# Kernel tuning notes

Hardware: AMD Instinct MI355X
Metric: run time of the kernel (lower is better)

Reference implementation:

```python
import jax, jax.numpy as jnp
import numpy as np

N = 20000      # nodes per side
E = 160000     # edges
C = 512        # input_channels
C_OUT = 512    # output_channels
TEMP = float(np.sqrt(C))  # self.temperature = sqrt(input_channels)
NEG_SLOPE = 0.01          # LeakyReLU default


def _xavier(key, shape):
    fan_in, fan_out = shape[1], shape[0]
    std = np.sqrt(2.0 / (fan_in + fan_out))
    return jax.random.normal(key, shape, dtype=jnp.float32) * std


def setup_inputs() -> dict:
    key = jax.random.key(0)
    ks = jax.random.split(key, 10)
    return {
        "node_left": jax.random.normal(ks[0], (N, C), dtype=jnp.float32),
        "segmentation_index_left": jax.random.randint(ks[1], (E,), 0, N),
        "index_left": jax.random.randint(ks[2], (E,), 0, N),
        "node_right": jax.random.normal(ks[3], (N, C), dtype=jnp.float32),
        "segmentation_index_right": jax.random.randint(ks[4], (E,), 0, N),
        "index_right": jax.random.randint(ks[5], (E,), 0, N),
        "Wk": _xavier(ks[6], (C, C)),      # key_projection.weight
        "Wv": _xavier(ks[7], (C, C)),      # value_projection.weight
        "Wo": _xavier(ks[8], (C_OUT, C)),  # out_projection Linear weight
        "bo": jnp.zeros((C_OUT,), dtype=jnp.float32),
    }


def segment_softmax(scores, seg_idx, num_segments, temperature):
    # numerically stable softmax over variable-length segments of edges
    s = scores / temperature
    m = jax.ops.segment_max(s, seg_idx, num_segments=num_segments)
    m = jnp.where(jnp.isneginf(m), 0.0, m)  # guard empty segments
    e = jnp.exp(s - m[seg_idx])
    z = jax.ops.segment_sum(e, seg_idx, num_segments=num_segments)
    return e / z[seg_idx]


def _message(translation, seg_idx, num_segments, neighbor, Wo, bo):
    attn = segment_softmax(translation, seg_idx, num_segments, TEMP)  # [E]
    # dropout is identity at inference
    msg = jax.ops.segment_sum(attn[:, None] * neighbor, seg_idx,
                              num_segments=num_segments)  # [N, C]
    h = msg @ Wo.T + bo
    return jnp.where(h >= 0, h, NEG_SLOPE * h)  # LeakyReLU


def reference(node_left, segmentation_index_left, index_left,
              node_right, segmentation_index_right, index_right,
              Wk, Wv, Wo, bo):
    n_left = node_left.shape[0]
    n_right = node_right.shape[0]
    # key projections gathered to edges
    left_center = (node_left @ Wk.T)[segmentation_index_left]    # [E, C]
    right_center = (node_right @ Wk.T)[segmentation_index_right]  # [E, C]
    # value projections gathered to edges (cross side)
    left_neighbor = (node_right @ Wv.T)[segmentation_index_right]  # [E, C]
    right_neighbor = (node_left @ Wv.T)[segmentation_index_left]   # [E, C]
    translation = jnp.sum(left_center * right_center, axis=1)      # [E]
    msg_left = _message(translation, segmentation_index_left, n_left,
                        left_neighbor, Wo, bo)
    msg_right = _message(translation, segmentation_index_right, n_right,
                         right_neighbor, Wo, bo)
    return (msg_left, msg_right)
```

## Files before the change

### kernel.cpp

```cpp
#include <hip/hip_runtime.h>


#define C_DIM 512
#define TEMP_INV (1.0f / 22.627416997969522f)

using bf16x8 = __attribute__((ext_vector_type(8))) __bf16;
using s16x8  = __attribute__((ext_vector_type(8))) short;
using s16x4  = __attribute__((ext_vector_type(4))) short;
using f32x4  = __attribute__((ext_vector_type(4))) float;

__device__ __forceinline__ float bf2f(short u) {
    union { unsigned u; float f; } t;
    t.u = ((unsigned)(unsigned short)u) << 16;
    return t.f;
}
__device__ __forceinline__ short f2bf(float f) {
    union { float f; unsigned u; } t;
    t.f = f;
    unsigned r = t.u + 0x7FFFu + ((t.u >> 16) & 1u);
    return (short)(r >> 16);
}

__global__ void cvt2_f32_bf16(const float* __restrict__ inA,
                              const float* __restrict__ inB,
                              short* __restrict__ out, long n4half) {
    long i = (long)blockIdx.x * blockDim.x + threadIdx.x;
    long stride = (long)gridDim.x * blockDim.x;
    long n4 = 2 * n4half;
    for (; i < n4; i += stride) {
        const float4* src = (i < n4half)
            ? reinterpret_cast<const float4*>(inA) + i
            : reinterpret_cast<const float4*>(inB) + (i - n4half);
        float4 v = *src;
        s16x4 o;
        o[0] = f2bf(v.x); o[1] = f2bf(v.y); o[2] = f2bf(v.z); o[3] = f2bf(v.w);
        reinterpret_cast<s16x4*>(out)[i] = o;
    }
}

__global__ void cvt_weights(const float* __restrict__ Wk,
                            const float* __restrict__ Wv,
                            const float* __restrict__ Wo,
                            short* __restrict__ Wkc, short* __restrict__ WoB,
                            short* __restrict__ WvT) {
    int b = blockIdx.x;
    int tid = threadIdx.x;
    if (b < 64) {
        __shared__ float t[64][65];
        int bx = b & 7, by = b >> 3;
#pragma unroll
        for (int i = 0; i < 4; ++i) {
            int idx = i * 256 + tid;
            int row = idx >> 4, c4 = idx & 15;
            float4 v = *(const float4*)&Wv[(size_t)(by * 64 + row) * 512 + bx * 64 + c4 * 4];
            t[row][c4 * 4 + 0] = v.x; t[row][c4 * 4 + 1] = v.y;
            t[row][c4 * 4 + 2] = v.z; t[row][c4 * 4 + 3] = v.w;
        }
        __syncthreads();
#pragma unroll
        for (int i = 0; i < 4; ++i) {
            int idx = i * 256 + tid;
            int row = idx >> 4, g = idx & 15;
            s16x4 o;
            o[0] = f2bf(t[g * 4 + 0][row]);
            o[1] = f2bf(t[g * 4 + 1][row]);
            o[2] = f2bf(t[g * 4 + 2][row]);
            o[3] = f2bf(t[g * 4 + 3][row]);
            *(s16x4*)&WvT[(size_t)(bx * 64 + row) * 512 + by * 64 + g * 4] = o;
        }
    } else {
        const float* src = (b < 128) ? Wk : Wo;
        short* dst = (b < 128) ? Wkc : WoB;
        long base = (long)(b & 63) * 1024;
#pragma unroll
        for (int i = 0; i < 4; ++i) {
            long idx = base + i * 256 + tid;
            float4 v = reinterpret_cast<const float4*>(src)[idx];
            s16x4 o;
            o[0] = f2bf(v.x); o[1] = f2bf(v.y); o[2] = f2bf(v.z); o[3] = f2bf(v.w);
            reinterpret_cast<s16x4*>(dst)[idx] = o;
        }
    }
}

__global__ __launch_bounds__(256, 3)
void gemm_bt(const short* __restrict__ A, const short* __restrict__ B,
             short* __restrict__ Cp, int M, int N, int K, int nn, int total) {
    __shared__ short As[3][128 * 32];
    __shared__ short Bs[3][128 * 32];

    const int bid = blockIdx.x;
    const int q = total >> 3, r = total & 7;
    const int xcd = bid & 7, idx = bid >> 3;
    const int swz = (xcd < r ? xcd * (q + 1) : r * (q + 1) + (xcd - r) * q) + idx;
    const int bm = (swz / nn) * 128;
    const int bn = (swz % nn) * 128;

    const int tid  = threadIdx.x;
    const int lane = tid & 63;
    const int wid  = tid >> 6;
    const int wm   = (wid >> 1) * 64;
    const int wn   = (wid & 1) * 64;
    const int lrow  = lane & 15;
    const int khalf = lane >> 4;

    auto stage = [&](short* dA, short* dB, int k0) {
#pragma unroll
        for (int j = 0; j < 2; ++j) {
            int L    = j * 256 + tid;
            int pr   = L >> 3;
            int slot = L & 7;
            int g    = slot ^ (pr & 7);
            int row  = pr * 2 + (g >> 2);
            int kg   = g & 3;
            int wb   = (j * 256 + (tid & ~63)) * 16;
            {
                int grow = bm + row; if (grow >= M) grow = M - 1;
                const short* src = A + (size_t)grow * K + k0 + kg * 8;
                __builtin_amdgcn_global_load_lds(
                    (__attribute__((address_space(1))) void*)src,
                    (__attribute__((address_space(3))) void*)((char*)dA + wb),
                    16, 0, 0);
            }
            {
                int grow = bn + row; if (grow >= N) grow = N - 1;
                const short* src = B + (size_t)grow * K + k0 + kg * 8;
                __builtin_amdgcn_global_load_lds(
                    (__attribute__((address_space(1))) void*)src,
                    (__attribute__((address_space(3))) void*)((char*)dB + wb),
                    16, 0, 0);
            }
        }
    };

    auto frag = [&](const short* h, int row) -> bf16x8 {
        int pr   = row >> 1;
        int g    = ((row & 1) << 2) | khalf;
        int slot = g ^ (pr & 7);
        return *(const bf16x8*)&h[pr * 64 + slot * 8];
    };

    f32x4 acc[4][4] = {};
    const int nt = K >> 5;

    stage(As[0], Bs[0], 0);
    stage(As[1], Bs[1], 32);

    for (int t = 0; t < nt; ++t) {
        const unsigned cur = (unsigned)t % 3u;
        if (t + 2 < nt) {
            const unsigned nxt = (unsigned)(t + 2) % 3u;
            stage(As[nxt], Bs[nxt], (t + 2) << 5);
            asm volatile("s_waitcnt vmcnt(8)" ::: "memory");
        } else if (t + 1 < nt) {
            asm volatile("s_waitcnt vmcnt(4)" ::: "memory");
        } else {
            asm volatile("s_waitcnt vmcnt(0)" ::: "memory");
        }
        __builtin_amdgcn_s_barrier();

        const short* as = As[cur];
        const short* bs = Bs[cur];
        bf16x8 af[4], bfr[4];
#pragma unroll
        for (int m = 0; m < 4; ++m) af[m] = frag(as, wm + m * 16 + lrow);
#pragma unroll
        for (int n = 0; n < 4; ++n) bfr[n] = frag(bs, wn + n * 16 + lrow);

        asm volatile("s_waitcnt lgkmcnt(0)" ::: "memory");
        __builtin_amdgcn_sched_barrier(0);
        __builtin_amdgcn_s_barrier();

        __builtin_amdgcn_s_setprio(1);
#pragma unroll
        for (int m = 0; m < 4; ++m)
#pragma unroll
            for (int n = 0; n < 4; ++n)
                acc[m][n] = __builtin_amdgcn_mfma_f32_16x16x32_bf16(
                    af[m], bfr[n], acc[m][n], 0, 0, 0);
        __builtin_amdgcn_s_setprio(0);
    }

    const int crow0 = (lane >> 4) * 4;
    const int ccol  = lane & 15;
#pragma unroll
    for (int m = 0; m < 4; ++m) {
#pragma unroll
        for (int n = 0; n < 4; ++n) {
            int col = bn + wn + n * 16 + ccol;
#pragma unroll
            for (int r2 = 0; r2 < 4; ++r2) {
                int row = bm + wm + m * 16 + crow0 + r2;
                if (row < M) Cp[(size_t)row * N + col] = f2bf(acc[m][n][r2]);
            }
        }
    }
}

__global__ void count_edges2(const int* __restrict__ segL, const int* __restrict__ segR,
                             int* __restrict__ cnt, int E, int N) {
    int i = blockIdx.x * blockDim.x + threadIdx.x;
    int st = gridDim.x * blockDim.x;
    for (; i < E; i += st) {
        atomicAdd(&cnt[segL[i]], 1);
        atomicAdd(&cnt[N + segR[i]], 1);
    }
}

__global__ void scan_blocks(const int* __restrict__ cnt, int* __restrict__ off,
                            int* __restrict__ bsum, int n) {
    __shared__ int ws[4];
    int tid = threadIdx.x, lane = tid & 63, wid = tid >> 6;
    int i = blockIdx.x * 256 + tid;
    int x = (i < n) ? cnt[i] : 0;
    int v = x;
#pragma unroll
    for (int d = 1; d < 64; d <<= 1) {
        int t = __shfl_up(v, d, 64);
        if (lane >= d) v += t;
    }
    if (lane == 63) ws[wid] = v;
    __syncthreads();
    int woff = 0;
    for (int w = 0; w < wid; ++w) woff += ws[w];
    v += woff;
    if (i < n) off[i + 1] = v;
    if (tid == 255) bsum[blockIdx.x] = v;
}

__global__ void scan_tops(int* __restrict__ bsum, int nb) {
    __shared__ int ws[4];
    int tid = threadIdx.x, lane = tid & 63, wid = tid >> 6;
    int x = (tid < nb) ? bsum[tid] : 0;
    int v = x;
#pragma unroll
    for (int d = 1; d < 64; d <<= 1) {
        int t = __shfl_up(v, d, 64);
        if (lane >= d) v += t;
    }
    if (lane == 63) ws[wid] = v;
    __syncthreads();
    int woff = 0;
    for (int w = 0; w < wid; ++w) woff += ws[w];
    v += woff;
    if (tid < nb) bsum[tid] = v - x;
}

__global__ void scan_apply(int* __restrict__ off, const int* __restrict__ bsum,
                           int* __restrict__ cnt, int n) {
    int i = blockIdx.x * 256 + threadIdx.x;
    if (i < n) {
        off[i + 1] += bsum[blockIdx.x];
        cnt[i] = 0;
    }
    if (i == 0) off[0] = 0;
}

__global__ void edge_dot_fill(const short* __restrict__ proj,
                              const int* __restrict__ segL, const int* __restrict__ segR,
                              const int* __restrict__ off, int* __restrict__ cur,
                              float2* __restrict__ pairs, int E, int N) {
    int e0 = blockIdx.x * 16 + (threadIdx.x >> 6) * 4;
    if (e0 >= E) return;
    int lane = threadIdx.x & 63;

    float sum[4];
#pragma unroll
    for (int k = 0; k < 4; ++k) {
        int ek = e0 + k; if (ek >= E) ek = e0;
        const short* a = proj + (size_t)segL[ek] * 1024 + lane * 8;
        const short* b = proj + (size_t)(N + segR[ek]) * 1024 + lane * 8;
        s16x8 va = *(const s16x8*)a;
        s16x8 vb = *(const s16x8*)b;
        float s = 0.f;
#pragma unroll
        for (int j = 0; j < 8; ++j) s += bf2f(va[j]) * bf2f(vb[j]);
        sum[k] = s;
    }
#pragma unroll
    for (int o = 32; o > 0; o >>= 1) {
#pragma unroll
        for (int k = 0; k < 4; ++k) sum[k] += __shfl_xor(sum[k], o, 64);
    }
    if (lane < 4) {
        int ek = e0 + lane;
        if (ek < E) {
            float s = (lane == 0) ? sum[0] : (lane == 1) ? sum[1]
                    : (lane == 2) ? sum[2] : sum[3];
            float we = __expf(s * TEMP_INV);
            int sl = segL[ek], sr = segR[ek];
            int pl = off[sl] + atomicAdd(&cur[sl], 1);
            pairs[pl] = make_float2(we, __int_as_float(N + sr));
            int pr = off[N + sr] + atomicAdd(&cur[N + sr], 1);
            pairs[pr] = make_float2(we, __int_as_float(sl));
        }
    }
}

__global__ void node_msg(const int* __restrict__ off,
                         const float2* __restrict__ pairs,
                         const short* __restrict__ proj,
                         const float* __restrict__ bo,
                         float* __restrict__ out, int NN2) {
    int n = blockIdx.x * 4 + (threadIdx.x >> 6);
    if (n >= NN2) return;
    int lane = threadIdx.x & 63;
    int beg = off[n], end = off[n + 1];
    const short* VW = proj + 512 + lane * 8;

    float acc[8] = {};
    float z = 0.f;
    int i = beg;
    for (; i + 3 < end; i += 4) {
        float2 p0 = pairs[i], p1 = pairs[i + 1];
        float2 p2 = pairs[i + 2], p3 = pairs[i + 3];
        const s16x8 v0 = *(const s16x8*)(VW + (size_t)__float_as_int(p0.y) * 1024);
        const s16x8 v1 = *(const s16x8*)(VW + (size_t)__float_as_int(p1.y) * 1024);
        const s16x8 v2 = *(const s16x8*)(VW + (size_t)__float_as_int(p2.y) * 1024);
        const s16x8 v3 = *(const s16x8*)(VW + (size_t)__float_as_int(p3.y) * 1024);
        z += (p0.x + p1.x) + (p2.x + p3.x);
#pragma unroll
        for (int j = 0; j < 8; ++j) {
            acc[j] += p0.x * bf2f(v0[j]) + p1.x * bf2f(v1[j]);
            acc[j] += p2.x * bf2f(v2[j]) + p3.x * bf2f(v3[j]);
        }
    }
    for (; i < end; ++i) {
        float2 p = pairs[i];
        const s16x8 v = *(const s16x8*)(VW + (size_t)__float_as_int(p.y) * 1024);
        z += p.x;
#pragma unroll
        for (int j = 0; j < 8; ++j) acc[j] += p.x * bf2f(v[j]);
    }
    float inv = (z > 0.f) ? 1.f / z : 0.f;

    float4 bs0 = *(const float4*)&bo[lane * 8];
    float4 bs1 = *(const float4*)&bo[lane * 8 + 4];
    float bb[8] = {bs0.x, bs0.y, bs0.z, bs0.w, bs1.x, bs1.y, bs1.z, bs1.w};
    f32x4 h0, h1;
#pragma unroll
    for (int j = 0; j < 4; ++j) {
        float v = acc[j] * inv + bb[j];
        h0[j] = v >= 0.f ? v : 0.01f * v;
    }
#pragma unroll
    for (int j = 0; j < 4; ++j) {
        float v = acc[4 + j] * inv + bb[4 + j];
        h1[j] = v >= 0.f ? v : 0.01f * v;
    }
    float* orow = out + (size_t)n * C_DIM + lane * 8;
    __builtin_nontemporal_store(h0, (f32x4*)&orow[0]);
    __builtin_nontemporal_store(h1, (f32x4*)&orow[4]);
}

extern "C" void kernel_launch(void* const* d_in, const int* in_sizes, int n_in,
                              void* d_out, int out_size, void* d_ws, size_t ws_size,
                              hipStream_t stream) {
    const float* node_left  = (const float*)d_in[0];
    const int*   segL       = (const int*)d_in[1];
    const float* node_right = (const float*)d_in[3];
    const int*   segR       = (const int*)d_in[4];
    const float* Wk         = (const float*)d_in[6];
    const float* Wv         = (const float*)d_in[7];
    const float* Wo         = (const float*)d_in[8];
    const float* bo         = (const float*)d_in[9];

    const int C = C_DIM;
    const int N = in_sizes[0] / C;
    const int E = in_sizes[1];
    const int NN2 = 2 * N;

    size_t offb = 0;
    auto alloc = [&](size_t bytes) -> void* {
        void* p = (char*)d_ws + offb;
        offb += (bytes + 255) & ~(size_t)255;
        return p;
    };
    short* nodeLR_b = (short*)alloc((size_t)NN2 * C * 2);
    short* Wkc_b  = (short*)alloc((size_t)1024 * C * 2);
    short* Wc_b   = Wkc_b + (size_t)C * C;
    short* Wo_b   = (short*)alloc((size_t)C * C * 2);
    short* WvT_b  = (short*)alloc((size_t)C * C * 2);
    short* proj   = (short*)alloc((size_t)NN2 * 1024 * 2);
    float2* pairs = (float2*)alloc((size_t)2 * E * 8);
    int* cnt  = (int*)alloc((size_t)NN2 * 4);
    int* off  = (int*)alloc((size_t)(NN2 + 1) * 4);
    int* bsum = (int*)alloc(256 * 4);

    const int nsb = (NN2 + 255) / 256;

    hipMemsetAsync(cnt, 0, (size_t)NN2 * 4, stream);
    count_edges2<<<512, 256, 0, stream>>>(segL, segR, cnt, E, N);
    scan_blocks<<<nsb, 256, 0, stream>>>(cnt, off, bsum, NN2);
    scan_tops<<<1, 256, 0, stream>>>(bsum, nsb);
    scan_apply<<<nsb, 256, 0, stream>>>(off, bsum, cnt, NN2);

    cvt2_f32_bf16<<<2048, 256, 0, stream>>>(node_left, node_right, nodeLR_b,
                                            (long)N * C / 4);
    cvt_weights<<<192, 256, 0, stream>>>(Wk, Wv, Wo, Wkc_b, Wo_b, WvT_b);

    gemm_bt<<<16, 256, 0, stream>>>(Wo_b, WvT_b, Wc_b, C, C, C, 4, 16);
    {
        int nm = (NN2 + 127) / 128, nn = 1024 / 128;
        int total = nm * nn;
        gemm_bt<<<total, 256, 0, stream>>>(nodeLR_b, Wkc_b, proj, NN2, 1024, C,
                                           nn, total);
    }

    edge_dot_fill<<<(E + 15) / 16, 256, 0, stream>>>(proj, segL, segR, off, cnt,
                                                     pairs, E, N);

    node_msg<<<(NN2 + 3) / 4, 256, 0, stream>>>(off, pairs, proj, bo,
                                                (float*)d_out, NN2);
}
```

Before: 230.1 us.

## Fold key projection into Gram matrix so only right side is projected

```diff
diff --git a/kernel.cpp b/kernel.cpp
--- a/kernel.cpp
+++ b/kernel.cpp
@@ -41,18 +41,21 @@
 __global__ void cvt_weights(const float* __restrict__ Wk,
                             const float* __restrict__ Wv,
                             const float* __restrict__ Wo,
-                            short* __restrict__ Wkc, short* __restrict__ WoB,
-                            short* __restrict__ WvT) {
+                            short* __restrict__ WkT, short* __restrict__ WvT,
+                            short* __restrict__ WoB) {
     int b = blockIdx.x;
     int tid = threadIdx.x;
-    if (b < 64) {
+    if (b < 128) {
+        const float* src = (b < 64) ? Wv : Wk;
+        short* dst = (b < 64) ? WvT : WkT;
+        int bb = b & 63;
         __shared__ float t[64][65];
-        int bx = b & 7, by = b >> 3;
+        int bx = bb & 7, by = bb >> 3;
 #pragma unroll
         for (int i = 0; i < 4; ++i) {
             int idx = i * 256 + tid;
             int row = idx >> 4, c4 = idx & 15;
-            float4 v = *(const float4*)&Wv[(size_t)(by * 64 + row) * 512 + bx * 64 + c4 * 4];
+            float4 v = *(const float4*)&src[(size_t)(by * 64 + row) * 512 + bx * 64 + c4 * 4];
             t[row][c4 * 4 + 0] = v.x; t[row][c4 * 4 + 1] = v.y;
             t[row][c4 * 4 + 2] = v.z; t[row][c4 * 4 + 3] = v.w;
         }
@@ -66,35 +69,40 @@
             o[1] = f2bf(t[g * 4 + 1][row]);
             o[2] = f2bf(t[g * 4 + 2][row]);
             o[3] = f2bf(t[g * 4 + 3][row]);
-            *(s16x4*)&WvT[(size_t)(bx * 64 + row) * 512 + by * 64 + g * 4] = o;
+            *(s16x4*)&dst[(size_t)(bx * 64 + row) * 512 + by * 64 + g * 4] = o;
         }
     } else {
-        const float* src = (b < 128) ? Wk : Wo;
-        short* dst = (b < 128) ? Wkc : WoB;
         long base = (long)(b & 63) * 1024;
 #pragma unroll
         for (int i = 0; i < 4; ++i) {
             long idx = base + i * 256 + tid;
-            float4 v = reinterpret_cast<const float4*>(src)[idx];
+            float4 v = reinterpret_cast<const float4*>(Wo)[idx];
             s16x4 o;
             o[0] = f2bf(v.x); o[1] = f2bf(v.y); o[2] = f2bf(v.z); o[3] = f2bf(v.w);
-            reinterpret_cast<s16x4*>(dst)[idx] = o;
-        }
-    }
-}
-
-__global__ __launch_bounds__(256, 3)
-void gemm_bt(const short* __restrict__ A, const short* __restrict__ B,
-             short* __restrict__ Cp, int M, int N, int K, int nn, int total) {
-    __shared__ short As[3][128 * 32];
-    __shared__ short Bs[3][128 * 32];
+            reinterpret_cast<s16x4*>(WoB)[idx] = o;
+        }
+    }
+}
+
+__global__ __launch_bounds__(256, 4)
+void gemm_dual(const short* __restrict__ A0, const short* __restrict__ B0,
+               short* __restrict__ C0, int M0, int t0,
+               const short* __restrict__ A1, const short* __restrict__ B1,
+               short* __restrict__ C1, int M1, int total) {
+    __shared__ short As[2][128 * 32];
+    __shared__ short Bs[2][128 * 32];
 
     const int bid = blockIdx.x;
     const int q = total >> 3, r = total & 7;
     const int xcd = bid & 7, idx = bid >> 3;
     const int swz = (xcd < r ? xcd * (q + 1) : r * (q + 1) + (xcd - r) * q) + idx;
-    const int bm = (swz / nn) * 128;
-    const int bn = (swz % nn) * 128;
+
+    const short* A; const short* B; short* Cp; int M; int tile;
+    if (swz < t0) { A = A0; B = B0; Cp = C0; M = M0; tile = swz; }
+    else          { A = A1; B = B1; Cp = C1; M = M1; tile = swz - t0; }
+    const int bm = (tile >> 2) * 128;
+    const int bn = (tile & 3) * 128;
+    const int K = C_DIM;
 
     const int tid  = threadIdx.x;
     const int lane = tid & 63;
@@ -123,7 +131,7 @@
                     16, 0, 0);
             }
             {
-                int grow = bn + row; if (grow >= N) grow = N - 1;
+                int grow = bn + row;
                 const short* src = B + (size_t)grow * K + k0 + kg * 8;
                 __builtin_amdgcn_global_load_lds(
                     (__attribute__((address_space(1))) void*)src,
@@ -144,15 +152,11 @@
     const int nt = K >> 5;
 
     stage(As[0], Bs[0], 0);
-    stage(As[1], Bs[1], 32);
 
     for (int t = 0; t < nt; ++t) {
-        const unsigned cur = (unsigned)t % 3u;
-        if (t + 2 < nt) {
-            const unsigned nxt = (unsigned)(t + 2) % 3u;
-            stage(As[nxt], Bs[nxt], (t + 2) << 5);
-            asm volatile("s_waitcnt vmcnt(8)" ::: "memory");
-        } else if (t + 1 < nt) {
+        const int cur = t & 1;
+        if (t + 1 < nt) {
+            stage(As[cur ^ 1], Bs[cur ^ 1], (t + 1) << 5);
             asm volatile("s_waitcnt vmcnt(4)" ::: "memory");
         } else {
             asm volatile("s_waitcnt vmcnt(0)" ::: "memory");
@@ -191,7 +195,7 @@
 #pragma unroll
             for (int r2 = 0; r2 < 4; ++r2) {
                 int row = bm + wm + m * 16 + crow0 + r2;
-                if (row < M) Cp[(size_t)row * N + col] = f2bf(acc[m][n][r2]);
+                if (row < M) Cp[(size_t)row * C_DIM + col] = f2bf(acc[m][n][r2]);
             }
         }
     }
@@ -256,7 +260,8 @@
     if (i == 0) off[0] = 0;
 }
 
-__global__ void edge_dot_fill(const short* __restrict__ proj,
+__global__ void edge_dot_fill(const short* __restrict__ KL,
+                              const short* __restrict__ KR,
                               const int* __restrict__ segL, const int* __restrict__ segR,
                               const int* __restrict__ off, int* __restrict__ cur,
                               float2* __restrict__ pairs, int E, int N) {
@@ -268,8 +273,8 @@
 #pragma unroll
     for (int k = 0; k < 4; ++k) {
         int ek = e0 + k; if (ek >= E) ek = e0;
-        const short* a = proj + (size_t)segL[ek] * 1024 + lane * 8;
-        const short* b = proj + (size_t)(N + segR[ek]) * 1024 + lane * 8;
+        const short* a = KL + (size_t)segL[ek] * 512 + lane * 8;
+        const short* b = KR + (size_t)segR[ek] * 512 + lane * 8;
         s16x8 va = *(const s16x8*)a;
         s16x8 vb = *(const s16x8*)b;
         float s = 0.f;
@@ -299,14 +304,14 @@
 
 __global__ void node_msg(const int* __restrict__ off,
                          const float2* __restrict__ pairs,
-                         const short* __restrict__ proj,
+                         const short* __restrict__ VW,
                          const float* __restrict__ bo,
                          float* __restrict__ out, int NN2) {
     int n = blockIdx.x * 4 + (threadIdx.x >> 6);
     if (n >= NN2) return;
     int lane = threadIdx.x & 63;
     int beg = off[n], end = off[n + 1];
-    const short* VW = proj + 512 + lane * 8;
+    const short* VWp = VW + lane * 8;
 
     float acc[8] = {};
     float z = 0.f;
@@ -314,10 +319,10 @@
     for (; i + 3 < end; i += 4) {
         float2 p0 = pairs[i], p1 = pairs[i + 1];
         float2 p2 = pairs[i + 2], p3 = pairs[i + 3];
-        const s16x8 v0 = *(const s16x8*)(VW + (size_t)__float_as_int(p0.y) * 1024);
-        const s16x8 v1 = *(const s16x8*)(VW + (size_t)__float_as_int(p1.y) * 1024);
-        const s16x8 v2 = *(const s16x8*)(VW + (size_t)__float_as_int(p2.y) * 1024);
-        const s16x8 v3 = *(const s16x8*)(VW + (size_t)__float_as_int(p3.y) * 1024);
+        const s16x8 v0 = *(const s16x8*)(VWp + (size_t)__float_as_int(p0.y) * 512);
+        const s16x8 v1 = *(const s16x8*)(VWp + (size_t)__float_as_int(p1.y) * 512);
+        const s16x8 v2 = *(const s16x8*)(VWp + (size_t)__float_as_int(p2.y) * 512);
+        const s16x8 v3 = *(const s16x8*)(VWp + (size_t)__float_as_int(p3.y) * 512);
         z += (p0.x + p1.x) + (p2.x + p3.x);
 #pragma unroll
         for (int j = 0; j < 8; ++j) {
@@ -327,7 +332,7 @@
     }
     for (; i < end; ++i) {
         float2 p = pairs[i];
-        const s16x8 v = *(const s16x8*)(VW + (size_t)__float_as_int(p.y) * 1024);
+        const s16x8 v = *(const s16x8*)(VWp + (size_t)__float_as_int(p.y) * 512);
         z += p.x;
 #pragma unroll
         for (int j = 0; j < 8; ++j) acc[j] += p.x * bf2f(v[j]);
@@ -377,11 +382,15 @@
         return p;
     };
     short* nodeLR_b = (short*)alloc((size_t)NN2 * C * 2);
-    short* Wkc_b  = (short*)alloc((size_t)1024 * C * 2);
-    short* Wc_b   = Wkc_b + (size_t)C * C;
-    short* Wo_b   = (short*)alloc((size_t)C * C * 2);
-    short* WvT_b  = (short*)alloc((size_t)C * C * 2);
-    short* proj   = (short*)alloc((size_t)NN2 * 1024 * 2);
+    short* nodeL_b  = nodeLR_b;
+    short* nodeR_b  = nodeLR_b + (size_t)N * C;
+    short* WkT_b = (short*)alloc((size_t)C * C * 2);
+    short* WvT_b = (short*)alloc((size_t)C * C * 2);
+    short* Wo_b  = (short*)alloc((size_t)C * C * 2);
+    short* Wc_b  = (short*)alloc((size_t)C * C * 2);
+    short* G_b   = (short*)alloc((size_t)C * C * 2);
+    short* VW    = (short*)alloc((size_t)NN2 * C * 2);
+    short* KR2   = (short*)alloc((size_t)N * C * 2);
     float2* pairs = (float2*)alloc((size_t)2 * E * 8);
     int* cnt  = (int*)alloc((size_t)NN2 * 4);
     int* off  = (int*)alloc((size_t)(NN2 + 1) * 4);
@@ -397,19 +406,21 @@
 
     cvt2_f32_bf16<<<2048, 256, 0, stream>>>(node_left, node_right, nodeLR_b,
                                             (long)N * C / 4);
-    cvt_weights<<<192, 256, 0, stream>>>(Wk, Wv, Wo, Wkc_b, Wo_b, WvT_b);
-
-    gemm_bt<<<16, 256, 0, stream>>>(Wo_b, WvT_b, Wc_b, C, C, C, 4, 16);
+    cvt_weights<<<192, 256, 0, stream>>>(Wk, Wv, Wo, WkT_b, WvT_b, Wo_b);
+
+    gemm_dual<<<32, 256, 0, stream>>>(Wo_b, WvT_b, Wc_b, C, 16,
+                                      WkT_b, WkT_b, G_b, C, 32);
+
     {
-        int nm = (NN2 + 127) / 128, nn = 1024 / 128;
-        int total = nm * nn;
-        gemm_bt<<<total, 256, 0, stream>>>(nodeLR_b, Wkc_b, proj, NN2, 1024, C,
-                                           nn, total);
-    }
-
-    edge_dot_fill<<<(E + 15) / 16, 256, 0, stream>>>(proj, segL, segR, off, cnt,
-                                                     pairs, E, N);
-
-    node_msg<<<(NN2 + 3) / 4, 256, 0, stream>>>(off, pairs, proj, bo,
+        int t0 = ((NN2 + 127) / 128) * 4;
+        int total = t0 + ((N + 127) / 128) * 4;
+        gemm_dual<<<total, 256, 0, stream>>>(nodeLR_b, Wc_b, VW, NN2, t0,
+                                             nodeR_b, G_b, KR2, N, total);
+    }
+
+    edge_dot_fill<<<(E + 15) / 16, 256, 0, stream>>>(nodeL_b, KR2, segL, segR,
+                                                     off, cnt, pairs, E, N);
+
+    node_msg<<<(NN2 + 3) / 4, 256, 0, stream>>>(off, pairs, VW, bo,
                                                 (float*)d_out, NN2);
 }
```

After: 211.6 us. -8.1%, faster.
